# Performance work log

Hardware: AMD Instinct MI355X
Metric: run time of the kernel (lower is better)

## Reference

```python
import jax, jax.numpy as jnp
import numpy as np

WINDOW_SIZE = 11
SIGMA = 1.5


def _make_window(channel):
    # 1D gaussian, normalized, then outer product -> (C, 1, K, K) depthwise kernel
    xs = np.arange(WINDOW_SIZE) - WINDOW_SIZE // 2
    g = np.exp(-(xs ** 2) / (2.0 * SIGMA ** 2))
    g = g / g.sum()
    w2d = np.outer(g, g).astype(np.float32)
    w = np.broadcast_to(w2d[None, None], (channel, 1, WINDOW_SIZE, WINDOW_SIZE))
    return jnp.asarray(np.ascontiguousarray(w))


def _dwconv(x, window, channel):
    # depthwise valid conv, NCHW layout, groups = channel
    return jax.lax.conv_general_dilated(
        x, window,
        window_strides=(1, 1), padding='VALID',
        dimension_numbers=('NCHW', 'OIHW', 'NCHW'),
        feature_group_count=channel)


def setup_inputs() -> dict:
    key = jax.random.key(0)
    k1, k2 = jax.random.split(key)
    img1 = jax.random.uniform(k1, (32, 3, 512, 512), dtype=jnp.float32)
    img2 = jax.random.uniform(k2, (32, 3, 512, 512), dtype=jnp.float32)
    return {"img1": img1, "img2": img2}


def reference(img1, img2):
    channel = img1.shape[1]
    window = _make_window(channel).astype(img1.dtype)

    # dynamic range heuristic (val_range is None in the module's usage)
    max_val = jnp.where(jnp.max(img1) > 128, 255.0, 1.0)
    min_val = jnp.where(jnp.min(img1) < -0.5, -1.0, 0.0)
    L = max_val - min_val

    mu1 = _dwconv(img1, window, channel)
    mu2 = _dwconv(img2, window, channel)
    mu1_sq = mu1 * mu1
    mu2_sq = mu2 * mu2
    mu1_mu2 = mu1 * mu2

    sigma1_sq = _dwconv(img1 * img1, window, channel) - mu1_sq
    sigma2_sq = _dwconv(img2 * img2, window, channel) - mu2_sq
    sigma12 = _dwconv(img1 * img2, window, channel) - mu1_mu2

    C1 = (0.01 * L) ** 2
    C2 = (0.03 * L) ** 2
    ssim_map = ((2 * mu1_mu2 + C1) * (2 * sigma12 + C2)) / (
        (mu1_sq + mu2_sq + C1) * (sigma1_sq + sigma2_sq + C2))
    return 1.0 - jnp.mean(ssim_map)
```

## Files before the change

kernel.cpp:

```cpp
#include <hip/hip_runtime.h>


constexpr int H   = 512;
constexpr int W   = 512;
constexpr int NCH = 96;
constexpr int KS  = 11;
constexpr int RAD = 5;
constexpr int HO  = 502;
constexpr int WO  = 502;
constexpr int TH  = 32;
constexpr int TW  = 116;
constexpr int RH  = 42;
constexpr int RW  = 128;
constexpr int NTX = 5;
constexpr int NTY = 16;

__device__ __forceinline__ unsigned fkey(float f) {
  unsigned u = __float_as_uint(f);
  return (u & 0x80000000u) ? ~u : (u | 0x80000000u);
}
__device__ __forceinline__ float funkey(unsigned k) {
  unsigned u = (k & 0x80000000u) ? (k & 0x7FFFFFFFu) : ~k;
  return __uint_as_float(u);
}

__global__ void init_ws_kernel(unsigned* ws) {
  ws[0] = 0u;
  ws[1] = 0xFFFFFFFFu;
  ((float*)ws)[2] = 0.0f;
}

__global__ __launch_bounds__(256) void minmax_kernel(
    const float4* __restrict__ x, unsigned* __restrict__ ws, int n4) {
  int tid = threadIdx.x;
  int gid = blockIdx.x * blockDim.x + tid;
  int stride = gridDim.x * blockDim.x;
  float mx = -3.4e38f, mn = 3.4e38f;
  for (int i = gid; i < n4; i += stride) {
    float4 v = x[i];
    mx = fmaxf(mx, fmaxf(fmaxf(v.x, v.y), fmaxf(v.z, v.w)));
    mn = fminf(mn, fminf(fminf(v.x, v.y), fminf(v.z, v.w)));
  }
  #pragma unroll
  for (int off = 32; off; off >>= 1) {
    mx = fmaxf(mx, __shfl_down(mx, off));
    mn = fminf(mn, __shfl_down(mn, off));
  }
  __shared__ float smx[4], smn[4];
  int lane = tid & 63, wid = tid >> 6;
  if (lane == 0) { smx[wid] = mx; smn[wid] = mn; }
  __syncthreads();
  if (tid == 0) {
    mx = fmaxf(fmaxf(smx[0], smx[1]), fmaxf(smx[2], smx[3]));
    mn = fminf(fminf(smn[0], smn[1]), fminf(smn[2], smn[3]));
    atomicMax(&ws[0], fkey(mx));
    atomicMin(&ws[1], fkey(mn));
  }
}

__global__ __launch_bounds__(256) void ssim_kernel(
    const float* __restrict__ img1, const float* __restrict__ img2,
    const unsigned* __restrict__ wsk, float* __restrict__ sum_out) {
  __shared__ __align__(16) float s1[RH][RW];
  __shared__ __align__(16) float s2[RH][RW];
  __shared__ __align__(16) float vr[8][5][RW];
  __shared__ float bsum[4];

  const int tid = threadIdx.x;
  const int tx = blockIdx.x, ty = blockIdx.y, pl = blockIdx.z;
  const int row0 = ty * TH, col0 = tx * TW;
  const float* p1 = img1 + (size_t)pl * H * W;
  const float* p2 = img2 + (size_t)pl * H * W;

  float gw[KS];
  {
    float s = 0.f;
    #pragma unroll
    for (int k = 0; k < KS; ++k) {
      float d = (float)(k - RAD);
      gw[k] = expf(-(d * d) * (1.0f / 4.5f));
      s += gw[k];
    }
    float inv = 1.0f / s;
    #pragma unroll
    for (int k = 0; k < KS; ++k) gw[k] *= inv;
  }

  const float maxv = funkey(wsk[0]);
  const float minv = funkey(wsk[1]);
  const float L = (maxv > 128.0f ? 255.0f : 1.0f) - (minv < -0.5f ? -1.0f : 0.0f);
  float C1 = 0.01f * L; C1 = C1 * C1;
  float C2 = 0.03f * L; C2 = C2 * C2;

  for (int idx = tid; idx < RH * 32; idx += 256) {
    int r = idx >> 5, c4 = idx & 31;
    int gr = row0 + r, gc = col0 + (c4 << 2);
    float4 a = make_float4(0.f, 0.f, 0.f, 0.f);
    float4 b = a;
    if (gr < H && gc < W) {
      a = *reinterpret_cast<const float4*>(p1 + gr * W + gc);
      b = *reinterpret_cast<const float4*>(p2 + gr * W + gc);
    }
    *reinterpret_cast<float4*>(&s1[r][c4 << 2]) = a;
    *reinterpret_cast<float4*>(&s2[r][c4 << 2]) = b;
  }
  __syncthreads();

  float lsum = 0.f;

  for (int p = 0; p < 4; ++p) {
    {
      const int half = tid >> 7;
      const int c = tid & 127;
      const int r0 = p * 8 + half * 4;
      float acc[4][5];
      #pragma unroll
      for (int dr = 0; dr < 4; ++dr)
        #pragma unroll
        for (int q = 0; q < 5; ++q) acc[dr][q] = 0.f;

      #pragma unroll
      for (int ir = 0; ir < 14; ++ir) {
        float a = s1[r0 + ir][c];
        float b = s2[r0 + ir][c];
        float aa = a * a, bb = b * b, ab = a * b;
        #pragma unroll
        for (int dr = 0; dr < 4; ++dr) {
          int k = ir - dr;
          if (k >= 0 && k < KS) {
            float w = gw[k];
            acc[dr][0] = fmaf(w, a,  acc[dr][0]);
            acc[dr][1] = fmaf(w, b,  acc[dr][1]);
            acc[dr][2] = fmaf(w, aa, acc[dr][2]);
            acc[dr][3] = fmaf(w, bb, acc[dr][3]);
            acc[dr][4] = fmaf(w, ab, acc[dr][4]);
          }
        }
      }
      #pragma unroll
      for (int dr = 0; dr < 4; ++dr)
        #pragma unroll
        for (int q = 0; q < 5; ++q)
          vr[half * 4 + dr][q][c] = acc[dr][q];
    }
    __syncthreads();

    {
      const int rh = tid >> 5;
      const int s  = tid & 31;
      if (s < 29) {
        float hv[5][4];
        #pragma unroll
        for (int q = 0; q < 5; ++q) {
          const float* vp = &vr[rh][q][s << 2];
          float4 A  = *reinterpret_cast<const float4*>(vp);
          float4 Bv = *reinterpret_cast<const float4*>(vp + 4);
          float4 Cv = *reinterpret_cast<const float4*>(vp + 8);
          float2 Dv = *reinterpret_cast<const float2*>(vp + 12);
          float v[14] = {A.x, A.y, A.z, A.w, Bv.x, Bv.y, Bv.z, Bv.w,
                         Cv.x, Cv.y, Cv.z, Cv.w, Dv.x, Dv.y};
          #pragma unroll
          for (int j = 0; j < 4; ++j) {
            float h = 0.f;
            #pragma unroll
            for (int k = 0; k < KS; ++k) h = fmaf(gw[k], v[j + k], h);
            hv[q][j] = h;
          }
        }
        const int orow = row0 + p * 8 + rh;
        #pragma unroll
        for (int j = 0; j < 4; ++j) {
          int ocol = col0 + (s << 2) + j;
          if (orow < HO && ocol < WO) {
            float mu1 = hv[0][j], mu2 = hv[1][j];
            float m11 = mu1 * mu1, m22 = mu2 * mu2, m12 = mu1 * mu2;
            float s11 = hv[2][j] - m11;
            float s22 = hv[3][j] - m22;
            float s12 = hv[4][j] - m12;
            float num = (2.f * m12 + C1) * (2.f * s12 + C2);
            float den = (m11 + m22 + C1) * (s11 + s22 + C2);
            lsum += num * __builtin_amdgcn_rcpf(den);
          }
        }
      }
    }
    __syncthreads();
  }

  #pragma unroll
  for (int off = 32; off; off >>= 1) lsum += __shfl_down(lsum, off);
  int lane = tid & 63, wid = tid >> 6;
  if (lane == 0) bsum[wid] = lsum;
  __syncthreads();
  if (tid == 0) atomicAdd(sum_out, bsum[0] + bsum[1] + bsum[2] + bsum[3]);
}

__global__ void finalize_kernel(const float* __restrict__ sum, float* __restrict__ out) {
  out[0] = 1.0f - sum[0] * (1.0f / 24192384.0f);
}

extern "C" void kernel_launch(void* const* d_in, const int* in_sizes, int n_in,
                              void* d_out, int out_size, void* d_ws, size_t ws_size,
                              hipStream_t stream) {
  const float* img1 = (const float*)d_in[0];
  const float* img2 = (const float*)d_in[1];
  float* out = (float*)d_out;
  unsigned* ws = (unsigned*)d_ws;

  init_ws_kernel<<<1, 1, 0, stream>>>(ws);

  int n4 = in_sizes[0] >> 2;
  minmax_kernel<<<1024, 256, 0, stream>>>((const float4*)img1, ws, n4);

  dim3 grid(NTX, NTY, NCH);
  ssim_kernel<<<grid, 256, 0, stream>>>(img1, img2, ws, (float*)ws + 2);

  finalize_kernel<<<1, 1, 0, stream>>>((const float*)ws + 2, out);
}
```

Before: 450.3 us.

## Stream rows through a register sliding window for the vertical Gaussian pass

Replaces the shared-memory tile staging with a column-per-thread streaming scheme. Each thread reads image rows straight from global memory and keeps 11 rolling vertical accumulators in registers, so each output row's vertical sum is produced once with no halo recomputation across row tiles. Only the vertically filtered rows go through shared memory for the horizontal pass. Blocks become taller (128 output rows) with 128 threads. This cuts redundant loads and FMAs but holds 55 accumulators per thread, which raises register pressure and lowers parallelism (fewer, longer blocks).

```diff
diff --git a/kernel.cpp b/kernel.cpp
--- a/kernel.cpp
+++ b/kernel.cpp
@@ -5,15 +5,15 @@
 constexpr int W   = 512;
 constexpr int NCH = 96;
 constexpr int KS  = 11;
-constexpr int RAD = 5;
 constexpr int HO  = 502;
 constexpr int WO  = 502;
-constexpr int TH  = 32;
-constexpr int TW  = 116;
-constexpr int RH  = 42;
-constexpr int RW  = 128;
-constexpr int NTX = 5;
-constexpr int NTY = 16;
+constexpr int PCOLS = 128;
+constexpr int OCOLS = 118;
+constexpr int OROWS = 128;
+constexpr int NG    = 13;
+constexpr int NBX   = 5;
+constexpr int NBY   = 4;
+constexpr int HPAD  = 132;
 
 __device__ __forceinline__ unsigned fkey(float f) {
   unsigned u = __float_as_uint(f);
@@ -58,17 +58,18 @@
   }
 }
 
-__global__ __launch_bounds__(256) void ssim_kernel(
+__global__ __launch_bounds__(128) void ssim_kernel(
     const float* __restrict__ img1, const float* __restrict__ img2,
     const unsigned* __restrict__ wsk, float* __restrict__ sum_out) {
-  __shared__ __align__(16) float s1[RH][RW];
-  __shared__ __align__(16) float s2[RH][RW];
-  __shared__ __align__(16) float vr[8][5][RW];
-  __shared__ float bsum[4];
+  __shared__ __align__(16) float hbuf[11][5][HPAD];
+  __shared__ float bsum[2];
 
   const int tid = threadIdx.x;
-  const int tx = blockIdx.x, ty = blockIdx.y, pl = blockIdx.z;
-  const int row0 = ty * TH, col0 = tx * TW;
+  const int bx = blockIdx.x, by = blockIdx.y, pl = blockIdx.z;
+  const int col0 = bx * OCOLS;
+  const int row0 = by * OROWS;
+  const int col  = col0 + tid;
+  const bool colok = (col < W);
   const float* p1 = img1 + (size_t)pl * H * W;
   const float* p2 = img2 + (size_t)pl * H * W;
 
@@ -77,7 +78,7 @@
     float s = 0.f;
     #pragma unroll
     for (int k = 0; k < KS; ++k) {
-      float d = (float)(k - RAD);
+      float d = (float)(k - 5);
       gw[k] = expf(-(d * d) * (1.0f / 4.5f));
       s += gw[k];
     }
@@ -92,67 +93,64 @@
   float C1 = 0.01f * L; C1 = C1 * C1;
   float C2 = 0.03f * L; C2 = C2 * C2;
 
-  for (int idx = tid; idx < RH * 32; idx += 256) {
-    int r = idx >> 5, c4 = idx & 31;
-    int gr = row0 + r, gc = col0 + (c4 << 2);
-    float4 a = make_float4(0.f, 0.f, 0.f, 0.f);
-    float4 b = a;
-    if (gr < H && gc < W) {
-      a = *reinterpret_cast<const float4*>(p1 + gr * W + gc);
-      b = *reinterpret_cast<const float4*>(p2 + gr * W + gc);
-    }
-    *reinterpret_cast<float4*>(&s1[r][c4 << 2]) = a;
-    *reinterpret_cast<float4*>(&s2[r][c4 << 2]) = b;
-  }
-  __syncthreads();
+  float acc[11][5];
+  #pragma unroll
+  for (int s = 0; s < 11; ++s)
+    #pragma unroll
+    for (int q = 0; q < 5; ++q) acc[s][q] = 0.f;
 
   float lsum = 0.f;
 
-  for (int p = 0; p < 4; ++p) {
-    {
-      const int half = tid >> 7;
-      const int c = tid & 127;
-      const int r0 = p * 8 + half * 4;
-      float acc[4][5];
+  #pragma unroll 1
+  for (int g = 0; g < NG; ++g) {
+    const int rbase = row0 + 11 * g;
+
+    float ra[11], rb[11];
+    #pragma unroll
+    for (int p = 0; p < 11; ++p) {
+      const int r = rbase + p;
+      const bool ok = colok && (r < H);
+      const float* a1 = p1 + (size_t)r * W + col;
+      const float* a2 = p2 + (size_t)r * W + col;
+      ra[p] = ok ? *a1 : 0.f;
+      rb[p] = ok ? *a2 : 0.f;
+    }
+
+    #pragma unroll
+    for (int p = 0; p < 11; ++p) {
+      const float a = ra[p], b = rb[p];
+      const float aa = a * a, bb = b * b, ab = a * b;
       #pragma unroll
-      for (int dr = 0; dr < 4; ++dr)
-        #pragma unroll
-        for (int q = 0; q < 5; ++q) acc[dr][q] = 0.f;
-
+      for (int s = 0; s < 11; ++s) {
+        const float w = gw[(p - s + 11) % 11];
+        acc[s][0] = fmaf(w, a,  acc[s][0]);
+        acc[s][1] = fmaf(w, b,  acc[s][1]);
+        acc[s][2] = fmaf(w, aa, acc[s][2]);
+        acc[s][3] = fmaf(w, bb, acc[s][3]);
+        acc[s][4] = fmaf(w, ab, acc[s][4]);
+      }
+      constexpr int ES[11] = {1,2,3,4,5,6,7,8,9,10,0};
+      const int es = ES[p];
       #pragma unroll
-      for (int ir = 0; ir < 14; ++ir) {
-        float a = s1[r0 + ir][c];
-        float b = s2[r0 + ir][c];
-        float aa = a * a, bb = b * b, ab = a * b;
-        #pragma unroll
-        for (int dr = 0; dr < 4; ++dr) {
-          int k = ir - dr;
-          if (k >= 0 && k < KS) {
-            float w = gw[k];
-            acc[dr][0] = fmaf(w, a,  acc[dr][0]);
-            acc[dr][1] = fmaf(w, b,  acc[dr][1]);
-            acc[dr][2] = fmaf(w, aa, acc[dr][2]);
-            acc[dr][3] = fmaf(w, bb, acc[dr][3]);
-            acc[dr][4] = fmaf(w, ab, acc[dr][4]);
-          }
-        }
+      for (int q = 0; q < 5; ++q) {
+        hbuf[p][q][tid] = acc[es][q];
+        acc[es][q] = 0.f;
       }
-      #pragma unroll
-      for (int dr = 0; dr < 4; ++dr)
-        #pragma unroll
-        for (int q = 0; q < 5; ++q)
-          vr[half * 4 + dr][q][c] = acc[dr][q];
     }
     __syncthreads();
 
-    {
-      const int rh = tid >> 5;
-      const int s  = tid & 31;
-      if (s < 29) {
+    #pragma unroll
+    for (int it = 0; it < 3; ++it) {
+      const int t  = it * 128 + tid;
+      const int rr = t >> 5;
+      const int sg = t & 31;
+      const int ol = 11 * g - 10 + rr;
+      const int orow = row0 + ol;
+      if (rr < 11 && sg < 30 && ol >= 0 && ol < OROWS && orow < HO) {
         float hv[5][4];
         #pragma unroll
         for (int q = 0; q < 5; ++q) {
-          const float* vp = &vr[rh][q][s << 2];
+          const float* vp = &hbuf[rr][q][sg << 2];
           float4 A  = *reinterpret_cast<const float4*>(vp);
           float4 Bv = *reinterpret_cast<const float4*>(vp + 4);
           float4 Cv = *reinterpret_cast<const float4*>(vp + 8);
@@ -167,11 +165,11 @@
             hv[q][j] = h;
           }
         }
-        const int orow = row0 + p * 8 + rh;
         #pragma unroll
         for (int j = 0; j < 4; ++j) {
-          int ocol = col0 + (s << 2) + j;
-          if (orow < HO && ocol < WO) {
+          const int oc = (sg << 2) + j;
+          const int ocol = col0 + oc;
+          if (oc < OCOLS && ocol < WO) {
             float mu1 = hv[0][j], mu2 = hv[1][j];
             float m11 = mu1 * mu1, m22 = mu2 * mu2, m12 = mu1 * mu2;
             float s11 = hv[2][j] - m11;
@@ -189,10 +187,10 @@
 
   #pragma unroll
   for (int off = 32; off; off >>= 1) lsum += __shfl_down(lsum, off);
-  int lane = tid & 63, wid = tid >> 6;
+  const int lane = tid & 63, wid = tid >> 6;
   if (lane == 0) bsum[wid] = lsum;
   __syncthreads();
-  if (tid == 0) atomicAdd(sum_out, bsum[0] + bsum[1] + bsum[2] + bsum[3]);
+  if (tid == 0) atomicAdd(sum_out, bsum[0] + bsum[1]);
 }
 
 __global__ void finalize_kernel(const float* __restrict__ sum, float* __restrict__ out) {
@@ -212,8 +210,8 @@
   int n4 = in_sizes[0] >> 2;
   minmax_kernel<<<1024, 256, 0, stream>>>((const float4*)img1, ws, n4);
 
-  dim3 grid(NTX, NTY, NCH);
-  ssim_kernel<<<grid, 256, 0, stream>>>(img1, img2, ws, (float*)ws + 2);
+  dim3 grid(NBX, NBY, NCH);
+  ssim_kernel<<<grid, 128, 0, stream>>>(img1, img2, ws, (float*)ws + 2);
 
   finalize_kernel<<<1, 1, 0, stream>>>((const float*)ws + 2, out);
 }
```

New measurement: 400.1 us. 11.1% less time.

## Rewrite SSIM as per-wave register-streaming separable filter with cross-lane permutes

Applied to the files above, without the earlier changes.

Replaces the shared-memory tiled SSIM kernel with a wave-level design. Each wavefront streams one 64-row band of one column strip, loading two columns per lane straight from global memory and prefetching the next row. The horizontal 11-tap pass gets its neighbours through ds_bpermute, and the vertical pass uses an 11-slot rotating accumulator ring held in registers. This removes LDS staging and block-wide barriers, at the cost of heavy register pressure (110 accumulators), redundant halo lanes, and per-row bpermute traffic. Gaussian weights now come from a constant table, and the min/max reduction is unrolled by four with a doubled grid.

```diff
diff --git a/kernel.cpp b/kernel.cpp
--- a/kernel.cpp
+++ b/kernel.cpp
@@ -1,19 +1,20 @@
 #include <hip/hip_runtime.h>
 
 
+constexpr int W   = 512;
 constexpr int H   = 512;
-constexpr int W   = 512;
 constexpr int NCH = 96;
-constexpr int KS  = 11;
-constexpr int RAD = 5;
-constexpr int HO  = 502;
 constexpr int WO  = 502;
-constexpr int TH  = 32;
-constexpr int TW  = 116;
-constexpr int RH  = 42;
-constexpr int RW  = 128;
-constexpr int NTX = 5;
-constexpr int NTY = 16;
+constexpr int SOUT = 118;
+constexpr int NSTRIP = 5;
+constexpr int ORB  = 64;
+constexpr int NBAND = 8;
+constexpr int NWAVE = NSTRIP * NBAND * NCH;
+
+__device__ __constant__ const float GW[11] = {
+  0.0010283885f, 0.0075987582f, 0.0360008058f, 0.1093606695f, 0.2130055279f,
+  0.2660116484f,
+  0.2130055279f, 0.1093606695f, 0.0360008058f, 0.0075987582f, 0.0010283885f};
 
 __device__ __forceinline__ unsigned fkey(float f) {
   unsigned u = __float_as_uint(f);
@@ -22,6 +23,9 @@
 __device__ __forceinline__ float funkey(unsigned k) {
   unsigned u = (k & 0x80000000u) ? (k & 0x7FFFFFFFu) : ~k;
   return __uint_as_float(u);
+}
+__device__ __forceinline__ float bperm(int byteidx, float v) {
+  return __int_as_float(__builtin_amdgcn_ds_bpermute(byteidx, __float_as_int(v)));
 }
 
 __global__ void init_ws_kernel(unsigned* ws) {
@@ -32,14 +36,23 @@
 
 __global__ __launch_bounds__(256) void minmax_kernel(
     const float4* __restrict__ x, unsigned* __restrict__ ws, int n4) {
-  int tid = threadIdx.x;
-  int gid = blockIdx.x * blockDim.x + tid;
-  int stride = gridDim.x * blockDim.x;
+  const int tid = threadIdx.x;
+  const int gid = blockIdx.x * 256 + tid;
+  const int S = gridDim.x * 256;
   float mx = -3.4e38f, mn = 3.4e38f;
-  for (int i = gid; i < n4; i += stride) {
-    float4 v = x[i];
-    mx = fmaxf(mx, fmaxf(fmaxf(v.x, v.y), fmaxf(v.z, v.w)));
-    mn = fminf(mn, fminf(fminf(v.x, v.y), fminf(v.z, v.w)));
+  for (int i = gid; i < n4; i += 4 * S) {
+    float4 v0 = x[i];
+    float4 v1 = (i + S     < n4) ? x[i + S]     : v0;
+    float4 v2 = (i + 2 * S < n4) ? x[i + 2 * S] : v0;
+    float4 v3 = (i + 3 * S < n4) ? x[i + 3 * S] : v0;
+    mx = fmaxf(mx, fmaxf(fmaxf(fmaxf(v0.x, v0.y), fmaxf(v0.z, v0.w)),
+                         fmaxf(fmaxf(v1.x, v1.y), fmaxf(v1.z, v1.w))));
+    mx = fmaxf(mx, fmaxf(fmaxf(fmaxf(v2.x, v2.y), fmaxf(v2.z, v2.w)),
+                         fmaxf(fmaxf(v3.x, v3.y), fmaxf(v3.z, v3.w))));
+    mn = fminf(mn, fminf(fminf(fminf(v0.x, v0.y), fminf(v0.z, v0.w)),
+                         fminf(fminf(v1.x, v1.y), fminf(v1.z, v1.w))));
+    mn = fminf(mn, fminf(fminf(fminf(v2.x, v2.y), fminf(v2.z, v2.w)),
+                         fminf(fminf(v3.x, v3.y), fminf(v3.z, v3.w))));
   }
   #pragma unroll
   for (int off = 32; off; off >>= 1) {
@@ -47,8 +60,8 @@
     mn = fminf(mn, __shfl_down(mn, off));
   }
   __shared__ float smx[4], smn[4];
-  int lane = tid & 63, wid = tid >> 6;
-  if (lane == 0) { smx[wid] = mx; smn[wid] = mn; }
+  const int lane = tid & 63, wib = tid >> 6;
+  if (lane == 0) { smx[wib] = mx; smn[wib] = mn; }
   __syncthreads();
   if (tid == 0) {
     mx = fmaxf(fmaxf(smx[0], smx[1]), fmaxf(smx[2], smx[3]));
@@ -61,136 +74,158 @@
 __global__ __launch_bounds__(256) void ssim_kernel(
     const float* __restrict__ img1, const float* __restrict__ img2,
     const unsigned* __restrict__ wsk, float* __restrict__ sum_out) {
-  __shared__ __align__(16) float s1[RH][RW];
-  __shared__ __align__(16) float s2[RH][RW];
-  __shared__ __align__(16) float vr[8][5][RW];
-  __shared__ float bsum[4];
-
-  const int tid = threadIdx.x;
-  const int tx = blockIdx.x, ty = blockIdx.y, pl = blockIdx.z;
-  const int row0 = ty * TH, col0 = tx * TW;
-  const float* p1 = img1 + (size_t)pl * H * W;
-  const float* p2 = img2 + (size_t)pl * H * W;
-
-  float gw[KS];
-  {
-    float s = 0.f;
-    #pragma unroll
-    for (int k = 0; k < KS; ++k) {
-      float d = (float)(k - RAD);
-      gw[k] = expf(-(d * d) * (1.0f / 4.5f));
-      s += gw[k];
-    }
-    float inv = 1.0f / s;
-    #pragma unroll
-    for (int k = 0; k < KS; ++k) gw[k] *= inv;
-  }
+  const int tid  = threadIdx.x;
+  const int lane = tid & 63;
+  const int wib  = tid >> 6;
+  const int wid  = blockIdx.x * 4 + wib;
+
+  const int strip = wid % NSTRIP;
+  const int band  = (wid / NSTRIP) % NBAND;
+  const int plane = wid / (NSTRIP * NBAND);
+
+  const int O0 = strip * SOUT;
+  const int r0 = band * ORB;
+  const int c0 = O0 + (lane << 1);
+  const bool cok = (c0 < W);
+
+  const float* p1 = img1 + (size_t)plane * (H * W);
+  const float* p2 = img2 + (size_t)plane * (H * W);
 
   const float maxv = funkey(wsk[0]);
   const float minv = funkey(wsk[1]);
   const float L = (maxv > 128.0f ? 255.0f : 1.0f) - (minv < -0.5f ? -1.0f : 0.0f);
-  float C1 = 0.01f * L; C1 = C1 * C1;
-  float C2 = 0.03f * L; C2 = C2 * C2;
-
-  for (int idx = tid; idx < RH * 32; idx += 256) {
-    int r = idx >> 5, c4 = idx & 31;
-    int gr = row0 + r, gc = col0 + (c4 << 2);
-    float4 a = make_float4(0.f, 0.f, 0.f, 0.f);
-    float4 b = a;
-    if (gr < H && gc < W) {
-      a = *reinterpret_cast<const float4*>(p1 + gr * W + gc);
-      b = *reinterpret_cast<const float4*>(p2 + gr * W + gc);
+  float C1 = 0.01f * L; C1 *= C1;
+  float C2 = 0.03f * L; C2 *= C2;
+
+  const int im3 = ((lane - 3) & 63) << 2;
+  const int im2 = ((lane - 2) & 63) << 2;
+  const int im1 = ((lane - 1) & 63) << 2;
+  const int ip1 = ((lane + 1) & 63) << 2;
+  const int ip2 = ((lane + 2) & 63) << 2;
+
+  float acc[11][5][2];
+  #pragma unroll
+  for (int s = 0; s < 11; ++s)
+    #pragma unroll
+    for (int q = 0; q < 5; ++q) { acc[s][q][0] = 0.f; acc[s][q][1] = 0.f; }
+
+  float lsum = 0.f;
+
+  float na0 = 0.f, na1 = 0.f, nb0 = 0.f, nb1 = 0.f;
+  if (cok) {
+    float2 t1 = *reinterpret_cast<const float2*>(p1 + (size_t)r0 * W + c0);
+    float2 t2 = *reinterpret_cast<const float2*>(p2 + (size_t)r0 * W + c0);
+    na0 = t1.x; na1 = t1.y; nb0 = t2.x; nb1 = t2.y;
+  }
+
+  #pragma unroll 1
+  for (int g = 0; g < 7; ++g) {
+    #pragma unroll
+    for (int p = 0; p < 11; ++p) {
+      const float ca0 = na0, ca1 = na1, cb0 = nb0, cb1 = nb1;
+
+      const int rn = r0 + 11 * g + p + 1;
+      if ((rn < H) && cok) {
+        float2 t1 = *reinterpret_cast<const float2*>(p1 + (size_t)rn * W + c0);
+        float2 t2 = *reinterpret_cast<const float2*>(p2 + (size_t)rn * W + c0);
+        na0 = t1.x; na1 = t1.y; nb0 = t2.x; nb1 = t2.y;
+      } else {
+        na0 = 0.f; na1 = 0.f; nb0 = 0.f; nb1 = 0.f;
+      }
+
+      float wa[12], wb[12];
+      wa[6] = ca0; wa[7] = ca1; wb[6] = cb0; wb[7] = cb1;
+      wa[0]  = bperm(im3, ca0); wa[1]  = bperm(im3, ca1);
+      wa[2]  = bperm(im2, ca0); wa[3]  = bperm(im2, ca1);
+      wa[4]  = bperm(im1, ca0); wa[5]  = bperm(im1, ca1);
+      wa[8]  = bperm(ip1, ca0); wa[9]  = bperm(ip1, ca1);
+      wa[10] = bperm(ip2, ca0); wa[11] = bperm(ip2, ca1);
+      wb[0]  = bperm(im3, cb0); wb[1]  = bperm(im3, cb1);
+      wb[2]  = bperm(im2, cb0); wb[3]  = bperm(im2, cb1);
+      wb[4]  = bperm(im1, cb0); wb[5]  = bperm(im1, cb1);
+      wb[8]  = bperm(ip1, cb0); wb[9]  = bperm(ip1, cb1);
+      wb[10] = bperm(ip2, cb0); wb[11] = bperm(ip2, cb1);
+
+      float h[5][2];
+      h[0][0] = 0.f; h[0][1] = 0.f; h[1][0] = 0.f; h[1][1] = 0.f;
+      #pragma unroll
+      for (int k = 0; k < 11; ++k) {
+        h[0][0] = fmaf(GW[k], wa[k],     h[0][0]);
+        h[0][1] = fmaf(GW[k], wa[k + 1], h[0][1]);
+        h[1][0] = fmaf(GW[k], wb[k],     h[1][0]);
+        h[1][1] = fmaf(GW[k], wb[k + 1], h[1][1]);
+      }
+      {
+        float sq[12];
+        #pragma unroll
+        for (int m = 0; m < 12; ++m) sq[m] = wa[m] * wa[m];
+        h[2][0] = 0.f; h[2][1] = 0.f;
+        #pragma unroll
+        for (int k = 0; k < 11; ++k) {
+          h[2][0] = fmaf(GW[k], sq[k],     h[2][0]);
+          h[2][1] = fmaf(GW[k], sq[k + 1], h[2][1]);
+        }
+      }
+      {
+        float sq[12];
+        #pragma unroll
+        for (int m = 0; m < 12; ++m) sq[m] = wb[m] * wb[m];
+        h[3][0] = 0.f; h[3][1] = 0.f;
+        #pragma unroll
+        for (int k = 0; k < 11; ++k) {
+          h[3][0] = fmaf(GW[k], sq[k],     h[3][0]);
+          h[3][1] = fmaf(GW[k], sq[k + 1], h[3][1]);
+        }
+      }
+      {
+        float sq[12];
+        #pragma unroll
+        for (int m = 0; m < 12; ++m) sq[m] = wa[m] * wb[m];
+        h[4][0] = 0.f; h[4][1] = 0.f;
+        #pragma unroll
+        for (int k = 0; k < 11; ++k) {
+          h[4][0] = fmaf(GW[k], sq[k],     h[4][0]);
+          h[4][1] = fmaf(GW[k], sq[k + 1], h[4][1]);
+        }
+      }
+
+      #pragma unroll
+      for (int s = 0; s < 11; ++s) {
+        const float wv = GW[(p - s + 11) % 11];
+        #pragma unroll
+        for (int q = 0; q < 5; ++q) {
+          acc[s][q][0] = fmaf(wv, h[q][0], acc[s][q][0]);
+          acc[s][q][1] = fmaf(wv, h[q][1], acc[s][q][1]);
+        }
+      }
+
+      const int es = (p + 1) % 11;
+      const int ol = 11 * g + p - 10;
+      const int orow = r0 + ol;
+      if (ol >= 0 && ol < ORB && orow < WO) {
+        #pragma unroll
+        for (int c = 0; c < 2; ++c) {
+          const int ocol = c0 - 6 + c;
+          const bool valid = (lane >= 3) && (lane <= 61) && (ocol < WO);
+          const float mu1 = acc[es][0][c], mu2 = acc[es][1][c];
+          const float m11 = mu1 * mu1, m22 = mu2 * mu2, m12 = mu1 * mu2;
+          const float s11 = acc[es][2][c] - m11;
+          const float s22 = acc[es][3][c] - m22;
+          const float s12 = acc[es][4][c] - m12;
+          const float num = (2.f * m12 + C1) * (2.f * s12 + C2);
+          const float den = (m11 + m22 + C1) * (s11 + s22 + C2);
+          lsum += valid ? num * __builtin_amdgcn_rcpf(den) : 0.f;
+        }
+      }
+      #pragma unroll
+      for (int q = 0; q < 5; ++q) { acc[es][q][0] = 0.f; acc[es][q][1] = 0.f; }
     }
-    *reinterpret_cast<float4*>(&s1[r][c4 << 2]) = a;
-    *reinterpret_cast<float4*>(&s2[r][c4 << 2]) = b;
-  }
-  __syncthreads();
-
-  float lsum = 0.f;
-
-  for (int p = 0; p < 4; ++p) {
-    {
-      const int half = tid >> 7;
-      const int c = tid & 127;
-      const int r0 = p * 8 + half * 4;
-      float acc[4][5];
-      #pragma unroll
-      for (int dr = 0; dr < 4; ++dr)
-        #pragma unroll
-        for (int q = 0; q < 5; ++q) acc[dr][q] = 0.f;
-
-      #pragma unroll
-      for (int ir = 0; ir < 14; ++ir) {
-        float a = s1[r0 + ir][c];
-        float b = s2[r0 + ir][c];
-        float aa = a * a, bb = b * b, ab = a * b;
-        #pragma unroll
-        for (int dr = 0; dr < 4; ++dr) {
-          int k = ir - dr;
-          if (k >= 0 && k < KS) {
-            float w = gw[k];
-            acc[dr][0] = fmaf(w, a,  acc[dr][0]);
-            acc[dr][1] = fmaf(w, b,  acc[dr][1]);
-            acc[dr][2] = fmaf(w, aa, acc[dr][2]);
-            acc[dr][3] = fmaf(w, bb, acc[dr][3]);
-            acc[dr][4] = fmaf(w, ab, acc[dr][4]);
-          }
-        }
-      }
-      #pragma unroll
-      for (int dr = 0; dr < 4; ++dr)
-        #pragma unroll
-        for (int q = 0; q < 5; ++q)
-          vr[half * 4 + dr][q][c] = acc[dr][q];
-    }
-    __syncthreads();
-
-    {
-      const int rh = tid >> 5;
-      const int s  = tid & 31;
-      if (s < 29) {
-        float hv[5][4];
-        #pragma unroll
-        for (int q = 0; q < 5; ++q) {
-          const float* vp = &vr[rh][q][s << 2];
-          float4 A  = *reinterpret_cast<const float4*>(vp);
-          float4 Bv = *reinterpret_cast<const float4*>(vp + 4);
-          float4 Cv = *reinterpret_cast<const float4*>(vp + 8);
-          float2 Dv = *reinterpret_cast<const float2*>(vp + 12);
-          float v[14] = {A.x, A.y, A.z, A.w, Bv.x, Bv.y, Bv.z, Bv.w,
-                         Cv.x, Cv.y, Cv.z, Cv.w, Dv.x, Dv.y};
-          #pragma unroll
-          for (int j = 0; j < 4; ++j) {
-            float h = 0.f;
-            #pragma unroll
-            for (int k = 0; k < KS; ++k) h = fmaf(gw[k], v[j + k], h);
-            hv[q][j] = h;
-          }
-        }
-        const int orow = row0 + p * 8 + rh;
-        #pragma unroll
-        for (int j = 0; j < 4; ++j) {
-          int ocol = col0 + (s << 2) + j;
-          if (orow < HO && ocol < WO) {
-            float mu1 = hv[0][j], mu2 = hv[1][j];
-            float m11 = mu1 * mu1, m22 = mu2 * mu2, m12 = mu1 * mu2;
-            float s11 = hv[2][j] - m11;
-            float s22 = hv[3][j] - m22;
-            float s12 = hv[4][j] - m12;
-            float num = (2.f * m12 + C1) * (2.f * s12 + C2);
-            float den = (m11 + m22 + C1) * (s11 + s22 + C2);
-            lsum += num * __builtin_amdgcn_rcpf(den);
-          }
-        }
-      }
-    }
-    __syncthreads();
   }
 
   #pragma unroll
   for (int off = 32; off; off >>= 1) lsum += __shfl_down(lsum, off);
-  int lane = tid & 63, wid = tid >> 6;
-  if (lane == 0) bsum[wid] = lsum;
+  __shared__ float bsum[4];
+  if (lane == 0) bsum[wib] = lsum;
   __syncthreads();
   if (tid == 0) atomicAdd(sum_out, bsum[0] + bsum[1] + bsum[2] + bsum[3]);
 }
@@ -210,10 +245,9 @@
   init_ws_kernel<<<1, 1, 0, stream>>>(ws);
 
   int n4 = in_sizes[0] >> 2;
-  minmax_kernel<<<1024, 256, 0, stream>>>((const float4*)img1, ws, n4);
-
-  dim3 grid(NTX, NTY, NCH);
-  ssim_kernel<<<grid, 256, 0, stream>>>(img1, img2, ws, (float*)ws + 2);
+  minmax_kernel<<<2048, 256, 0, stream>>>((const float4*)img1, ws, n4);
+
+  ssim_kernel<<<NWAVE / 4, 256, 0, stream>>>(img1, img2, ws, (float*)ws + 2);
 
   finalize_kernel<<<1, 1, 0, stream>>>((const float*)ws + 2, out);
 }
```

New measurement: 425.1 us. 5.6% less time.
